# Optimization experiments

Hardware: AMD Instinct MI355X
Metric: run time of the kernel (lower is better)

The kernel has to match this reference:

```python
import jax, jax.numpy as jnp
import numpy as np

ALPHA = 1.702  # sigmoid-GLU scale
LIMIT = 7.0    # clamp limit
TOP_K = 2      # num_experts_per_tok


def setup_inputs() -> dict:
    key = jax.random.key(0)
    ks = jax.random.split(key, 4)
    B, S, H, E, I = 2, 1024, 1024, 8, 2048
    return {
        "hidden_states": jax.random.normal(ks[0], (B, S, H), jnp.float32),
        "router_weight": jax.random.normal(ks[1], (E, H), jnp.float32),
        "router_bias": jnp.zeros((E,), jnp.float32),
        "gate_up_proj": jax.random.normal(ks[2], (E, H, 2 * I), jnp.float32) * 0.02,
        "gate_up_bias": jnp.zeros((E, 2 * I), jnp.float32),
        "down_proj": jax.random.normal(ks[3], (E, I, H), jnp.float32) * 0.02,
        "down_bias": jnp.zeros((E, H), jnp.float32),
    }


def reference(hidden_states, router_weight, router_bias, gate_up_proj,
              gate_up_bias, down_proj, down_bias):
    B, S, H = hidden_states.shape
    E, _, two_I = gate_up_proj.shape
    I = two_I // 2

    flat = hidden_states.reshape(B * S, H)  # [T, H]

    # Router: softmax + top-k
    logits = flat @ router_weight.T + router_bias            # [T, E]
    scores = jax.nn.softmax(logits, axis=-1)
    topk_w, topk_idx = jax.lax.top_k(scores, TOP_K)          # [T, K]

    # Dense per-expert gated FFN (einsum 'abmh,ehn->abemn' computes all experts
    # on all tokens; the reshape/permute dance is a mathematical no-op).
    gu = jnp.einsum('th,ehn->ten', flat, gate_up_proj) + gate_up_bias  # [T, E, 2I]
    gate = jnp.minimum(gu[..., :I], LIMIT)
    up = jnp.clip(gu[..., I:], -LIMIT, LIMIT)
    glu = gate * jax.nn.sigmoid(gate * ALPHA)
    act = (up + 1.0) * glu                                   # [T, E, I]

    down = jnp.einsum('tei,eih->teh', act, down_proj) + down_bias  # [T, E, H]

    # Combine: gather each token's top-k expert outputs, weighted sum.
    gathered = jnp.take_along_axis(down, topk_idx[:, :, None], axis=1)  # [T, K, H]
    out = (gathered * topk_w[:, :, None]).sum(axis=1)        # [T, H]
    return out.reshape(B, S, H)
```

## Files before the change

kernel.cpp:

```cpp
#include <hip/hip_runtime.h>
#include <math.h>

#define TT 2048
#define HH 1024
#define EE 8
#define II 2048
#define N1 4096
#define ALPHA 1.702f
#define LIMIT 7.0f

typedef __attribute__((ext_vector_type(8))) short short8;
typedef __attribute__((ext_vector_type(4))) float floatx4;
typedef __attribute__((ext_vector_type(4))) unsigned int uintx4;

__device__ __forceinline__ short f2bf(float f) {
  union { float f; unsigned u; } v; v.f = f;
  unsigned r = (v.u + 0x7fffu + ((v.u >> 16) & 1u)) >> 16;
  return (short)r;
}
__device__ __forceinline__ float bf2f(unsigned short s) {
  union { unsigned u; float f; } v; v.u = ((unsigned)s) << 16;
  return v.f;
}
__device__ __forceinline__ unsigned cvt2(float lo, float hi) {
  unsigned r;
  asm("v_cvt_pk_bf16_f32 %0, %1, %2" : "=v"(r) : "v"(lo), "v"(hi));
  return r;
}

__global__ __launch_bounds__(256) void router_kernel(
    const float* __restrict__ x, const float* __restrict__ rw,
    const float* __restrict__ rb, int* __restrict__ topk_idx,
    float* __restrict__ topk_w) {
  const int t = blockIdx.x;
  const float* xr = x + (size_t)t * HH;
  const int lane = threadIdx.x & 63;
  const int wave = threadIdx.x >> 6;
  float xv[16];
#pragma unroll
  for (int i = 0; i < 16; i++) xv[i] = xr[lane + i * 64];
  __shared__ float logits[EE];
#pragma unroll
  for (int ee = 0; ee < 2; ee++) {
    const int e = wave * 2 + ee;
    const float* wr = rw + (size_t)e * HH;
    float s = 0.f;
#pragma unroll
    for (int i = 0; i < 16; i++) s += xv[i] * wr[lane + i * 64];
#pragma unroll
    for (int off = 32; off > 0; off >>= 1) s += __shfl_down(s, off, 64);
    if (lane == 0) logits[e] = s + rb[e];
  }
  __syncthreads();
  if (threadIdx.x == 0) {
    float l[EE], sc[EE];
    float mx = -3.4e38f;
    for (int i = 0; i < EE; i++) { l[i] = logits[i]; mx = fmaxf(mx, l[i]); }
    float sum = 0.f;
    for (int i = 0; i < EE; i++) { sc[i] = expf(l[i] - mx); sum += sc[i]; }
    const float inv = 1.f / sum;
    int i0 = 0;
    for (int i = 1; i < EE; i++) if (sc[i] > sc[i0]) i0 = i;
    int i1 = (i0 == 0) ? 1 : 0;
    for (int i = 0; i < EE; i++) if (i != i0 && sc[i] > sc[i1]) i1 = i;
    topk_idx[t * 2 + 0] = i0;
    topk_idx[t * 2 + 1] = i1;
    topk_w[t * 2 + 0] = sc[i0] * inv;
    topk_w[t * 2 + 1] = sc[i1] * inv;
  }
}

__global__ void assign_kernel(const int* __restrict__ topk_idx,
                              int* __restrict__ counts, int* __restrict__ rows) {
  const int id = blockIdx.x * blockDim.x + threadIdx.x;
  if (id >= TT * 2) return;
  const int e = topk_idx[id];
  const int slot = atomicAdd(&counts[e], 1);
  rows[e * TT + slot] = id;
}

__global__ __launch_bounds__(512, 4) void gemm_gu(
    const float* __restrict__ x, const float* __restrict__ gup,
    const float* __restrict__ gub, const int* __restrict__ counts,
    const int* __restrict__ rows, unsigned short* __restrict__ gu) {
  const int e = blockIdx.z, mtile = blockIdx.y, ntile = blockIdx.x;
  const int count = counts[e];
  if (mtile * 128 >= count) return;
  const int* rl = rows + e * TT + mtile * 128;
  __shared__ short As[128][40];
  __shared__ short Bs[128][40];
  const int tid = threadIdx.x;
  const int lane = tid & 63, wave = tid >> 6;
  const int wm = (wave & 1) << 6, wn = (wave >> 1) << 5;
  const int quad = lane >> 4, r16 = lane & 15;

  const int arow = tid >> 2, akoct = tid & 3;
  const int cr = (mtile * 128 + arow < count) ? arow : (count - 1 - mtile * 128);
  const float* ap = x + (size_t)(rl[cr] >> 1) * HH + akoct * 8;

  const int bn = tid & 127, bko = tid >> 7;
  const float* bp = gup + (size_t)e * HH * N1 + (size_t)bko * 8 * N1 + ntile * 128 + bn;

  floatx4 acc[4][2] = {};

  float4 va0 = ((const float4*)ap)[0];
  float4 va1 = ((const float4*)ap)[1];
  float vb[8];
#pragma unroll
  for (int j = 0; j < 8; j++) vb[j] = bp[(size_t)j * N1];
  ap += 32;
  bp += (size_t)32 * N1;

  for (int k0 = 0; k0 < HH; k0 += 32) {
    __syncthreads();
    uintx4 aw, bw;
    aw[0] = cvt2(va0.x, va0.y); aw[1] = cvt2(va0.z, va0.w);
    aw[2] = cvt2(va1.x, va1.y); aw[3] = cvt2(va1.z, va1.w);
    bw[0] = cvt2(vb[0], vb[1]); bw[1] = cvt2(vb[2], vb[3]);
    bw[2] = cvt2(vb[4], vb[5]); bw[3] = cvt2(vb[6], vb[7]);
    *(uintx4*)&As[arow][akoct * 8] = aw;
    *(uintx4*)&Bs[bn][bko * 8] = bw;
    if (k0 + 32 < HH) {
      va0 = ((const float4*)ap)[0];
      va1 = ((const float4*)ap)[1];
#pragma unroll
      for (int j = 0; j < 8; j++) vb[j] = bp[(size_t)j * N1];
      ap += 32;
      bp += (size_t)32 * N1;
    }
    __syncthreads();
    short8 af[4], bf_[2];
#pragma unroll
    for (int i = 0; i < 4; i++)
      af[i] = *(const short8*)&As[wm + i * 16 + r16][quad * 8];
#pragma unroll
    for (int j = 0; j < 2; j++)
      bf_[j] = *(const short8*)&Bs[wn + j * 16 + r16][quad * 8];
#pragma unroll
    for (int i = 0; i < 4; i++)
#pragma unroll
      for (int j = 0; j < 2; j++)
        acc[i][j] = __builtin_amdgcn_mfma_f32_16x16x32_bf16(af[i], bf_[j], acc[i][j], 0, 0, 0);
  }
#pragma unroll
  for (int i = 0; i < 4; i++) {
#pragma unroll
    for (int reg = 0; reg < 4; reg++) {
      const int rrow = wm + i * 16 + quad * 4 + reg;
      if (mtile * 128 + rrow < count) {
        const int ent = rl[rrow];
        unsigned short* orow = gu + (size_t)ent * N1 + ntile * 128;
#pragma unroll
        for (int j = 0; j < 2; j++) {
          const int c = wn + j * 16 + r16;
          const float v = acc[i][j][reg] + gub[e * N1 + ntile * 128 + c];
          orow[c] = (unsigned short)f2bf(v);
        }
      }
    }
  }
}

__global__ void act_kernel(const unsigned short* __restrict__ gu,
                           unsigned short* __restrict__ act) {
  const int id = blockIdx.x * blockDim.x + threadIdx.x;
  const int r = id >> 8;
  const int i8 = (id & 255) * 8;
  short8 g8 = *(const short8*)(gu + (size_t)r * N1 + i8);
  short8 u8 = *(const short8*)(gu + (size_t)r * N1 + II + i8);
  short8 o;
#pragma unroll
  for (int j = 0; j < 8; j++) {
    float g = bf2f((unsigned short)g8[j]);
    float u = bf2f((unsigned short)u8[j]);
    g = fminf(g, LIMIT);
    u = fminf(fmaxf(u, -LIMIT), LIMIT);
    const float glu = g / (1.f + expf(-g * ALPHA));
    o[j] = f2bf((u + 1.f) * glu);
  }
  *(short8*)(act + (size_t)r * II + i8) = o;
}

__global__ __launch_bounds__(512, 4) void gemm_down(
    const unsigned short* __restrict__ act, const float* __restrict__ dp,
    const float* __restrict__ db, const int* __restrict__ counts,
    const int* __restrict__ rows, float* __restrict__ dout0,
    float* __restrict__ dout1) {
  const int e = blockIdx.z >> 1, kc = blockIdx.z & 1;
  const int mtile = blockIdx.y, ntile = blockIdx.x;
  const int count = counts[e];
  if (mtile * 128 >= count) return;
  const int kb = kc * (II / 2);
  const int* rl = rows + e * TT + mtile * 128;
  __shared__ short As[128][40];
  __shared__ short Bs[128][40];
  const int tid = threadIdx.x;
  const int lane = tid & 63, wave = tid >> 6;
  const int wm = (wave & 1) << 6, wn = (wave >> 1) << 5;
  const int quad = lane >> 4, r16 = lane & 15;

  const int arow = tid >> 2, akoct = tid & 3;
  const int cr = (mtile * 128 + arow < count) ? arow : (count - 1 - mtile * 128);
  const unsigned short* ap = act + (size_t)rl[cr] * II + kb + akoct * 8;

  const int bn = tid & 127, bko = tid >> 7;
  const float* bp = dp + (size_t)e * II * HH + (size_t)(kb + bko * 8) * HH + ntile * 128 + bn;

  floatx4 acc[4][2] = {};

  short8 va = *(const short8*)ap;
  float vb[8];
#pragma unroll
  for (int j = 0; j < 8; j++) vb[j] = bp[(size_t)j * HH];
  ap += 32;
  bp += (size_t)32 * HH;

  for (int k0 = 0; k0 < II / 2; k0 += 32) {
    __syncthreads();
    uintx4 bw;
    bw[0] = cvt2(vb[0], vb[1]); bw[1] = cvt2(vb[2], vb[3]);
    bw[2] = cvt2(vb[4], vb[5]); bw[3] = cvt2(vb[6], vb[7]);
    *(short8*)&As[arow][akoct * 8] = va;
    *(uintx4*)&Bs[bn][bko * 8] = bw;
    if (k0 + 32 < II / 2) {
      va = *(const short8*)ap;
#pragma unroll
      for (int j = 0; j < 8; j++) vb[j] = bp[(size_t)j * HH];
      ap += 32;
      bp += (size_t)32 * HH;
    }
    __syncthreads();
    short8 af[4], bf_[2];
#pragma unroll
    for (int i = 0; i < 4; i++)
      af[i] = *(const short8*)&As[wm + i * 16 + r16][quad * 8];
#pragma unroll
    for (int j = 0; j < 2; j++)
      bf_[j] = *(const short8*)&Bs[wn + j * 16 + r16][quad * 8];
#pragma unroll
    for (int i = 0; i < 4; i++)
#pragma unroll
      for (int j = 0; j < 2; j++)
        acc[i][j] = __builtin_amdgcn_mfma_f32_16x16x32_bf16(af[i], bf_[j], acc[i][j], 0, 0, 0);
  }
  float* dc = kc ? dout1 : dout0;
#pragma unroll
  for (int i = 0; i < 4; i++) {
#pragma unroll
    for (int reg = 0; reg < 4; reg++) {
      const int rrow = wm + i * 16 + quad * 4 + reg;
      if (mtile * 128 + rrow < count) {
        const int ent = rl[rrow];
        float* orow = dc + (size_t)ent * HH + ntile * 128;
#pragma unroll
        for (int j = 0; j < 2; j++) {
          const int c = wn + j * 16 + r16;
          float v = acc[i][j][reg];
          if (kc == 0) v += db[e * HH + ntile * 128 + c];
          orow[c] = v;
        }
      }
    }
  }
}

__global__ void combine_kernel(const float* __restrict__ d0,
                               const float* __restrict__ d1,
                               const float* __restrict__ tw,
                               float* __restrict__ out) {
  const int id = blockIdx.x * blockDim.x + threadIdx.x;
  const int t = id >> 8;
  const int h = (id & 255) * 4;
  const float w0 = tw[t * 2], w1 = tw[t * 2 + 1];
  const size_t r0 = (size_t)(2 * t) * HH + h;
  const size_t r1 = (size_t)(2 * t + 1) * HH + h;
  const float4 a0 = *(const float4*)(d0 + r0);
  const float4 a1 = *(const float4*)(d1 + r0);
  const float4 b0 = *(const float4*)(d0 + r1);
  const float4 b1 = *(const float4*)(d1 + r1);
  float4 o;
  o.x = w0 * (a0.x + a1.x) + w1 * (b0.x + b1.x);
  o.y = w0 * (a0.y + a1.y) + w1 * (b0.y + b1.y);
  o.z = w0 * (a0.z + a1.z) + w1 * (b0.z + b1.z);
  o.w = w0 * (a0.w + a1.w) + w1 * (b0.w + b1.w);
  *(float4*)(out + (size_t)t * HH + h) = o;
}

extern "C" void kernel_launch(void* const* d_in, const int* in_sizes, int n_in,
                              void* d_out, int out_size, void* d_ws, size_t ws_size,
                              hipStream_t stream) {
  const float* x   = (const float*)d_in[0];
  const float* rw  = (const float*)d_in[1];
  const float* rb  = (const float*)d_in[2];
  const float* gup = (const float*)d_in[3];
  const float* gub = (const float*)d_in[4];
  const float* dp  = (const float*)d_in[5];
  const float* db  = (const float*)d_in[6];
  float* out = (float*)d_out;

  char* ws = (char*)d_ws;
  int*   topk_idx = (int*)(ws + 0);
  float* topk_w   = (float*)(ws + 16384);
  int*   counts   = (int*)(ws + 32768);
  int*   rows     = (int*)(ws + 33024);
  unsigned short* gu  = (unsigned short*)(ws + 131072);
  unsigned short* act = (unsigned short*)(ws + 131072 + 33554432);
  float* dout0 = (float*)(ws + 131072 + 33554432 + 16777216);
  float* dout1 = (float*)(ws + 131072);

  router_kernel<<<TT, 256, 0, stream>>>(x, rw, rb, topk_idx, topk_w);
  hipMemsetAsync(counts, 0, 64, stream);
  assign_kernel<<<(TT * 2 + 255) / 256, 256, 0, stream>>>(topk_idx, counts, rows);
  gemm_gu<<<dim3(N1 / 128, TT / 128, EE), 512, 0, stream>>>(x, gup, gub, counts, rows, gu);
  act_kernel<<<(TT * 2 * II / 8) / 256, 256, 0, stream>>>(gu, act);
  gemm_down<<<dim3(HH / 128, TT / 128, EE * 2), 512, 0, stream>>>(act, dp, db, counts, rows, dout0, dout1);
  combine_kernel<<<(TT * HH / 4) / 256, 256, 0, stream>>>(dout0, dout1, topk_w, out);
}
```

Before: 399.7 us.

## Fuse GLU activation into gate/up GEMM and double-buffer LDS in both GEMMs

The gate/up GEMM now tiles matching gate and up columns together, 64 of each per block, so each block can apply the clamp, sigmoid-GLU and bf16 conversion in its epilogue. This removes the separate activation kernel and the bf16 gate/up intermediate round-trip through global memory. Both GEMMs also gain double-buffered LDS with one barrier per half-step, lighter lgkmcnt barriers and s_setprio around the MFMA bursts, to overlap global loads with compute. The cost is more LDS per block and more live registers, which may lower occupancy.

```diff
diff --git a/kernel.cpp b/kernel.cpp
--- a/kernel.cpp
+++ b/kernel.cpp
@@ -27,6 +27,8 @@
   asm("v_cvt_pk_bf16_f32 %0, %1, %2" : "=v"(r) : "v"(lo), "v"(hi));
   return r;
 }
+
+#define LDS_BARRIER() asm volatile("s_waitcnt lgkmcnt(0)\ns_barrier" ::: "memory")
 
 __global__ __launch_bounds__(256) void router_kernel(
     const float* __restrict__ x, const float* __restrict__ rw,
@@ -79,69 +81,104 @@
   rows[e * TT + slot] = id;
 }
 
-__global__ __launch_bounds__(512, 4) void gemm_gu(
+__global__ __launch_bounds__(512, 4) void gemm_gu_fused(
     const float* __restrict__ x, const float* __restrict__ gup,
     const float* __restrict__ gub, const int* __restrict__ counts,
-    const int* __restrict__ rows, unsigned short* __restrict__ gu) {
+    const int* __restrict__ rows, unsigned short* __restrict__ act) {
   const int e = blockIdx.z, mtile = blockIdx.y, ntile = blockIdx.x;
   const int count = counts[e];
   if (mtile * 128 >= count) return;
   const int* rl = rows + e * TT + mtile * 128;
-  __shared__ short As[128][40];
-  __shared__ short Bs[128][40];
+  __shared__ short As[2][128][40];
+  __shared__ short Bg[2][64][40];
+  __shared__ short Bu[2][64][40];
   const int tid = threadIdx.x;
   const int lane = tid & 63, wave = tid >> 6;
-  const int wm = (wave & 1) << 6, wn = (wave >> 1) << 5;
+  const int wm = (wave & 1) << 6, wn = (wave >> 1) << 4;
   const int quad = lane >> 4, r16 = lane & 15;
 
   const int arow = tid >> 2, akoct = tid & 3;
   const int cr = (mtile * 128 + arow < count) ? arow : (count - 1 - mtile * 128);
-  const float* ap = x + (size_t)(rl[cr] >> 1) * HH + akoct * 8;
-
-  const int bn = tid & 127, bko = tid >> 7;
-  const float* bp = gup + (size_t)e * HH * N1 + (size_t)bko * 8 * N1 + ntile * 128 + bn;
-
-  floatx4 acc[4][2] = {};
-
-  float4 va0 = ((const float4*)ap)[0];
-  float4 va1 = ((const float4*)ap)[1];
-  float vb[8];
-#pragma unroll
-  for (int j = 0; j < 8; j++) vb[j] = bp[(size_t)j * N1];
-  ap += 32;
-  bp += (size_t)32 * N1;
-
-  for (int k0 = 0; k0 < HH; k0 += 32) {
-    __syncthreads();
-    uintx4 aw, bw;
-    aw[0] = cvt2(va0.x, va0.y); aw[1] = cvt2(va0.z, va0.w);
-    aw[2] = cvt2(va1.x, va1.y); aw[3] = cvt2(va1.z, va1.w);
-    bw[0] = cvt2(vb[0], vb[1]); bw[1] = cvt2(vb[2], vb[3]);
-    bw[2] = cvt2(vb[4], vb[5]); bw[3] = cvt2(vb[6], vb[7]);
-    *(uintx4*)&As[arow][akoct * 8] = aw;
-    *(uintx4*)&Bs[bn][bko * 8] = bw;
-    if (k0 + 32 < HH) {
-      va0 = ((const float4*)ap)[0];
-      va1 = ((const float4*)ap)[1];
-#pragma unroll
-      for (int j = 0; j < 8; j++) vb[j] = bp[(size_t)j * N1];
-      ap += 32;
-      bp += (size_t)32 * N1;
+  const float* abase = x + (size_t)(rl[cr] >> 1) * HH + akoct * 8;
+
+  const int half = tid >> 8;
+  const int bn = tid & 63, bko = (tid >> 6) & 3;
+  const float* bbase = gup + (size_t)e * HH * N1 + (size_t)(bko * 8) * N1 +
+                       (size_t)half * II + ntile * 64 + bn;
+  short* bdst0 = half ? &Bu[0][bn][bko * 8] : &Bg[0][bn][bko * 8];
+  short* bdst1 = half ? &Bu[1][bn][bko * 8] : &Bg[1][bn][bko * 8];
+
+  floatx4 acc_g[4] = {{0.f,0.f,0.f,0.f},{0.f,0.f,0.f,0.f},{0.f,0.f,0.f,0.f},{0.f,0.f,0.f,0.f}};
+  floatx4 acc_u[4] = {{0.f,0.f,0.f,0.f},{0.f,0.f,0.f,0.f},{0.f,0.f,0.f,0.f},{0.f,0.f,0.f,0.f}};
+
+  const float* apA = abase;
+  const float* apB = abase + 32;
+  const float* bpA = bbase;
+  const float* bpB = bbase + (size_t)32 * N1;
+
+  float4 vaA0, vaA1, vaB0, vaB1;
+  float vbA0, vbA1, vbA2, vbA3, vbA4, vbA5, vbA6, vbA7;
+  float vbB0, vbB1, vbB2, vbB3, vbB4, vbB5, vbB6, vbB7;
+
+#define GU_LOADA() do { \
+  vaA0 = ((const float4*)apA)[0]; vaA1 = ((const float4*)apA)[1]; \
+  vbA0 = bpA[0]; vbA1 = bpA[(size_t)1 * N1]; vbA2 = bpA[(size_t)2 * N1]; vbA3 = bpA[(size_t)3 * N1]; \
+  vbA4 = bpA[(size_t)4 * N1]; vbA5 = bpA[(size_t)5 * N1]; vbA6 = bpA[(size_t)6 * N1]; vbA7 = bpA[(size_t)7 * N1]; \
+  apA += 64; bpA += (size_t)64 * N1; } while (0)
+#define GU_LOADB() do { \
+  vaB0 = ((const float4*)apB)[0]; vaB1 = ((const float4*)apB)[1]; \
+  vbB0 = bpB[0]; vbB1 = bpB[(size_t)1 * N1]; vbB2 = bpB[(size_t)2 * N1]; vbB3 = bpB[(size_t)3 * N1]; \
+  vbB4 = bpB[(size_t)4 * N1]; vbB5 = bpB[(size_t)5 * N1]; vbB6 = bpB[(size_t)6 * N1]; vbB7 = bpB[(size_t)7 * N1]; \
+  apB += 64; bpB += (size_t)64 * N1; } while (0)
+#define GU_CVTW(buf, va0, va1, b0, b1, b2, b3, b4, b5, b6, b7) do { \
+  uintx4 aw, bw; \
+  aw[0] = cvt2(va0.x, va0.y); aw[1] = cvt2(va0.z, va0.w); \
+  aw[2] = cvt2(va1.x, va1.y); aw[3] = cvt2(va1.z, va1.w); \
+  bw[0] = cvt2(b0, b1); bw[1] = cvt2(b2, b3); \
+  bw[2] = cvt2(b4, b5); bw[3] = cvt2(b6, b7); \
+  *(uintx4*)&As[buf][arow][akoct * 8] = aw; \
+  *(uintx4*)((buf) ? bdst1 : bdst0) = bw; } while (0)
+#define GU_MMA(buf) do { \
+  short8 af0 = *(const short8*)&As[buf][wm + 0 * 16 + r16][quad * 8]; \
+  short8 af1 = *(const short8*)&As[buf][wm + 1 * 16 + r16][quad * 8]; \
+  short8 af2 = *(const short8*)&As[buf][wm + 2 * 16 + r16][quad * 8]; \
+  short8 af3 = *(const short8*)&As[buf][wm + 3 * 16 + r16][quad * 8]; \
+  short8 bgf = *(const short8*)&Bg[buf][wn + r16][quad * 8]; \
+  short8 buf_ = *(const short8*)&Bu[buf][wn + r16][quad * 8]; \
+  __builtin_amdgcn_s_setprio(1); \
+  acc_g[0] = __builtin_amdgcn_mfma_f32_16x16x32_bf16(af0, bgf, acc_g[0], 0, 0, 0); \
+  acc_u[0] = __builtin_amdgcn_mfma_f32_16x16x32_bf16(af0, buf_, acc_u[0], 0, 0, 0); \
+  acc_g[1] = __builtin_amdgcn_mfma_f32_16x16x32_bf16(af1, bgf, acc_g[1], 0, 0, 0); \
+  acc_u[1] = __builtin_amdgcn_mfma_f32_16x16x32_bf16(af1, buf_, acc_u[1], 0, 0, 0); \
+  acc_g[2] = __builtin_amdgcn_mfma_f32_16x16x32_bf16(af2, bgf, acc_g[2], 0, 0, 0); \
+  acc_u[2] = __builtin_amdgcn_mfma_f32_16x16x32_bf16(af2, buf_, acc_u[2], 0, 0, 0); \
+  acc_g[3] = __builtin_amdgcn_mfma_f32_16x16x32_bf16(af3, bgf, acc_g[3], 0, 0, 0); \
+  acc_u[3] = __builtin_amdgcn_mfma_f32_16x16x32_bf16(af3, buf_, acc_u[3], 0, 0, 0); \
+  __builtin_amdgcn_s_setprio(0); } while (0)
+
+  GU_LOADA();
+  GU_LOADB();
+  GU_CVTW(0, vaA0, vaA1, vbA0, vbA1, vbA2, vbA3, vbA4, vbA5, vbA6, vbA7);
+  GU_LOADA();
+
+  const int NT = HH / 32;
+#pragma unroll 1
+  for (int t = 0; t < NT; t += 2) {
+    LDS_BARRIER();
+    GU_CVTW(1, vaB0, vaB1, vbB0, vbB1, vbB2, vbB3, vbB4, vbB5, vbB6, vbB7);
+    if (t + 3 < NT) GU_LOADB();
+    GU_MMA(0);
+    LDS_BARRIER();
+    if (t + 2 < NT) {
+      GU_CVTW(0, vaA0, vaA1, vbA0, vbA1, vbA2, vbA3, vbA4, vbA5, vbA6, vbA7);
+      if (t + 4 < NT) GU_LOADA();
     }
-    __syncthreads();
-    short8 af[4], bf_[2];
-#pragma unroll
-    for (int i = 0; i < 4; i++)
-      af[i] = *(const short8*)&As[wm + i * 16 + r16][quad * 8];
-#pragma unroll
-    for (int j = 0; j < 2; j++)
-      bf_[j] = *(const short8*)&Bs[wn + j * 16 + r16][quad * 8];
-#pragma unroll
-    for (int i = 0; i < 4; i++)
-#pragma unroll
-      for (int j = 0; j < 2; j++)
-        acc[i][j] = __builtin_amdgcn_mfma_f32_16x16x32_bf16(af[i], bf_[j], acc[i][j], 0, 0, 0);
-  }
+    GU_MMA(1);
+  }
+
+  const int nc = ntile * 64 + wn + r16;
+  const float bg_bias = gub[e * N1 + nc];
+  const float bu_bias = gub[e * N1 + II + nc];
 #pragma unroll
   for (int i = 0; i < 4; i++) {
 #pragma unroll
@@ -149,36 +186,19 @@
       const int rrow = wm + i * 16 + quad * 4 + reg;
       if (mtile * 128 + rrow < count) {
         const int ent = rl[rrow];
-        unsigned short* orow = gu + (size_t)ent * N1 + ntile * 128;
-#pragma unroll
-        for (int j = 0; j < 2; j++) {
-          const int c = wn + j * 16 + r16;
-          const float v = acc[i][j][reg] + gub[e * N1 + ntile * 128 + c];
-          orow[c] = (unsigned short)f2bf(v);
-        }
+        float g = acc_g[i][reg] + bg_bias;
+        float u = acc_u[i][reg] + bu_bias;
+        g = fminf(g, LIMIT);
+        u = fminf(fmaxf(u, -LIMIT), LIMIT);
+        const float glu = g / (1.f + expf(-g * ALPHA));
+        act[(size_t)ent * II + nc] = (unsigned short)f2bf((u + 1.f) * glu);
       }
     }
   }
-}
-
-__global__ void act_kernel(const unsigned short* __restrict__ gu,
-                           unsigned short* __restrict__ act) {
-  const int id = blockIdx.x * blockDim.x + threadIdx.x;
-  const int r = id >> 8;
-  const int i8 = (id & 255) * 8;
-  short8 g8 = *(const short8*)(gu + (size_t)r * N1 + i8);
-  short8 u8 = *(const short8*)(gu + (size_t)r * N1 + II + i8);
-  short8 o;
-#pragma unroll
-  for (int j = 0; j < 8; j++) {
-    float g = bf2f((unsigned short)g8[j]);
-    float u = bf2f((unsigned short)u8[j]);
-    g = fminf(g, LIMIT);
-    u = fminf(fmaxf(u, -LIMIT), LIMIT);
-    const float glu = g / (1.f + expf(-g * ALPHA));
-    o[j] = f2bf((u + 1.f) * glu);
-  }
-  *(short8*)(act + (size_t)r * II + i8) = o;
+#undef GU_LOADA
+#undef GU_LOADB
+#undef GU_CVTW
+#undef GU_MMA
 }
 
 __global__ __launch_bounds__(512, 4) void gemm_down(
@@ -192,8 +212,8 @@
   if (mtile * 128 >= count) return;
   const int kb = kc * (II / 2);
   const int* rl = rows + e * TT + mtile * 128;
-  __shared__ short As[128][40];
-  __shared__ short Bs[128][40];
+  __shared__ short As[2][128][40];
+  __shared__ short Bs[2][128][40];
   const int tid = threadIdx.x;
   const int lane = tid & 63, wave = tid >> 6;
   const int wm = (wave & 1) << 6, wn = (wave >> 1) << 5;
@@ -201,48 +221,77 @@
 
   const int arow = tid >> 2, akoct = tid & 3;
   const int cr = (mtile * 128 + arow < count) ? arow : (count - 1 - mtile * 128);
-  const unsigned short* ap = act + (size_t)rl[cr] * II + kb + akoct * 8;
+  const unsigned short* abase = act + (size_t)rl[cr] * II + kb + akoct * 8;
 
   const int bn = tid & 127, bko = tid >> 7;
-  const float* bp = dp + (size_t)e * II * HH + (size_t)(kb + bko * 8) * HH + ntile * 128 + bn;
+  const float* bbase = dp + (size_t)e * II * HH + (size_t)(kb + bko * 8) * HH +
+                       ntile * 128 + bn;
 
   floatx4 acc[4][2] = {};
 
-  short8 va = *(const short8*)ap;
-  float vb[8];
-#pragma unroll
-  for (int j = 0; j < 8; j++) vb[j] = bp[(size_t)j * HH];
-  ap += 32;
-  bp += (size_t)32 * HH;
-
-  for (int k0 = 0; k0 < II / 2; k0 += 32) {
-    __syncthreads();
-    uintx4 bw;
-    bw[0] = cvt2(vb[0], vb[1]); bw[1] = cvt2(vb[2], vb[3]);
-    bw[2] = cvt2(vb[4], vb[5]); bw[3] = cvt2(vb[6], vb[7]);
-    *(short8*)&As[arow][akoct * 8] = va;
-    *(uintx4*)&Bs[bn][bko * 8] = bw;
-    if (k0 + 32 < II / 2) {
-      va = *(const short8*)ap;
-#pragma unroll
-      for (int j = 0; j < 8; j++) vb[j] = bp[(size_t)j * HH];
-      ap += 32;
-      bp += (size_t)32 * HH;
+  const unsigned short* apA = abase;
+  const unsigned short* apB = abase + 32;
+  const float* bpA = bbase;
+  const float* bpB = bbase + (size_t)32 * HH;
+
+  short8 svA, svB;
+  float vbA0, vbA1, vbA2, vbA3, vbA4, vbA5, vbA6, vbA7;
+  float vbB0, vbB1, vbB2, vbB3, vbB4, vbB5, vbB6, vbB7;
+
+#define DN_LOADA() do { \
+  svA = *(const short8*)apA; \
+  vbA0 = bpA[0]; vbA1 = bpA[(size_t)1 * HH]; vbA2 = bpA[(size_t)2 * HH]; vbA3 = bpA[(size_t)3 * HH]; \
+  vbA4 = bpA[(size_t)4 * HH]; vbA5 = bpA[(size_t)5 * HH]; vbA6 = bpA[(size_t)6 * HH]; vbA7 = bpA[(size_t)7 * HH]; \
+  apA += 64; bpA += (size_t)64 * HH; } while (0)
+#define DN_LOADB() do { \
+  svB = *(const short8*)apB; \
+  vbB0 = bpB[0]; vbB1 = bpB[(size_t)1 * HH]; vbB2 = bpB[(size_t)2 * HH]; vbB3 = bpB[(size_t)3 * HH]; \
+  vbB4 = bpB[(size_t)4 * HH]; vbB5 = bpB[(size_t)5 * HH]; vbB6 = bpB[(size_t)6 * HH]; vbB7 = bpB[(size_t)7 * HH]; \
+  apB += 64; bpB += (size_t)64 * HH; } while (0)
+#define DN_CVTW(buf, sv, b0, b1, b2, b3, b4, b5, b6, b7) do { \
+  uintx4 bw; \
+  bw[0] = cvt2(b0, b1); bw[1] = cvt2(b2, b3); \
+  bw[2] = cvt2(b4, b5); bw[3] = cvt2(b6, b7); \
+  *(short8*)&As[buf][arow][akoct * 8] = sv; \
+  *(uintx4*)&Bs[buf][bn][bko * 8] = bw; } while (0)
+#define DN_MMA(buf) do { \
+  short8 af0 = *(const short8*)&As[buf][wm + 0 * 16 + r16][quad * 8]; \
+  short8 af1 = *(const short8*)&As[buf][wm + 1 * 16 + r16][quad * 8]; \
+  short8 af2 = *(const short8*)&As[buf][wm + 2 * 16 + r16][quad * 8]; \
+  short8 af3 = *(const short8*)&As[buf][wm + 3 * 16 + r16][quad * 8]; \
+  short8 bf0 = *(const short8*)&Bs[buf][wn + 0 * 16 + r16][quad * 8]; \
+  short8 bf1 = *(const short8*)&Bs[buf][wn + 1 * 16 + r16][quad * 8]; \
+  __builtin_amdgcn_s_setprio(1); \
+  acc[0][0] = __builtin_amdgcn_mfma_f32_16x16x32_bf16(af0, bf0, acc[0][0], 0, 0, 0); \
+  acc[0][1] = __builtin_amdgcn_mfma_f32_16x16x32_bf16(af0, bf1, acc[0][1], 0, 0, 0); \
+  acc[1][0] = __builtin_amdgcn_mfma_f32_16x16x32_bf16(af1, bf0, acc[1][0], 0, 0, 0); \
+  acc[1][1] = __builtin_amdgcn_mfma_f32_16x16x32_bf16(af1, bf1, acc[1][1], 0, 0, 0); \
+  acc[2][0] = __builtin_amdgcn_mfma_f32_16x16x32_bf16(af2, bf0, acc[2][0], 0, 0, 0); \
+  acc[2][1] = __builtin_amdgcn_mfma_f32_16x16x32_bf16(af2, bf1, acc[2][1], 0, 0, 0); \
+  acc[3][0] = __builtin_amdgcn_mfma_f32_16x16x32_bf16(af3, bf0, acc[3][0], 0, 0, 0); \
+  acc[3][1] = __builtin_amdgcn_mfma_f32_16x16x32_bf16(af3, bf1, acc[3][1], 0, 0, 0); \
+  __builtin_amdgcn_s_setprio(0); } while (0)
+
+  DN_LOADA();
+  DN_LOADB();
+  DN_CVTW(0, svA, vbA0, vbA1, vbA2, vbA3, vbA4, vbA5, vbA6, vbA7);
+  DN_LOADA();
+
+  const int NT = (II / 2) / 32;
+#pragma unroll 1
+  for (int t = 0; t < NT; t += 2) {
+    LDS_BARRIER();
+    DN_CVTW(1, svB, vbB0, vbB1, vbB2, vbB3, vbB4, vbB5, vbB6, vbB7);
+    if (t + 3 < NT) DN_LOADB();
+    DN_MMA(0);
+    LDS_BARRIER();
+    if (t + 2 < NT) {
+      DN_CVTW(0, svA, vbA0, vbA1, vbA2, vbA3, vbA4, vbA5, vbA6, vbA7);
+      if (t + 4 < NT) DN_LOADA();
     }
-    __syncthreads();
-    short8 af[4], bf_[2];
-#pragma unroll
-    for (int i = 0; i < 4; i++)
-      af[i] = *(const short8*)&As[wm + i * 16 + r16][quad * 8];
-#pragma unroll
-    for (int j = 0; j < 2; j++)
-      bf_[j] = *(const short8*)&Bs[wn + j * 16 + r16][quad * 8];
-#pragma unroll
-    for (int i = 0; i < 4; i++)
-#pragma unroll
-      for (int j = 0; j < 2; j++)
-        acc[i][j] = __builtin_amdgcn_mfma_f32_16x16x32_bf16(af[i], bf_[j], acc[i][j], 0, 0, 0);
-  }
+    DN_MMA(1);
+  }
+
   float* dc = kc ? dout1 : dout0;
 #pragma unroll
   for (int i = 0; i < 4; i++) {
@@ -262,6 +311,10 @@
       }
     }
   }
+#undef DN_LOADA
+#undef DN_LOADB
+#undef DN_CVTW
+#undef DN_MMA
 }
 
 __global__ void combine_kernel(const float* __restrict__ d0,
@@ -303,16 +356,14 @@
   float* topk_w   = (float*)(ws + 16384);
   int*   counts   = (int*)(ws + 32768);
   int*   rows     = (int*)(ws + 33024);
-  unsigned short* gu  = (unsigned short*)(ws + 131072);
-  unsigned short* act = (unsigned short*)(ws + 131072 + 33554432);
-  float* dout0 = (float*)(ws + 131072 + 33554432 + 16777216);
-  float* dout1 = (float*)(ws + 131072);
+  unsigned short* act = (unsigned short*)(ws + 131072);
+  float* dout0 = (float*)(ws + 131072 + 16777216);
+  float* dout1 = (float*)(ws + 131072 + 2 * 16777216);
 
   router_kernel<<<TT, 256, 0, stream>>>(x, rw, rb, topk_idx, topk_w);
   hipMemsetAsync(counts, 0, 64, stream);
   assign_kernel<<<(TT * 2 + 255) / 256, 256, 0, stream>>>(topk_idx, counts, rows);
-  gemm_gu<<<dim3(N1 / 128, TT / 128, EE), 512, 0, stream>>>(x, gup, gub, counts, rows, gu);
-  act_kernel<<<(TT * 2 * II / 8) / 256, 256, 0, stream>>>(gu, act);
+  gemm_gu_fused<<<dim3(II / 64, TT / 128, EE), 512, 0, stream>>>(x, gup, gub, counts, rows, act);
   gemm_down<<<dim3(HH / 128, TT / 128, EE * 2), 512, 0, stream>>>(act, dp, db, counts, rows, dout0, dout1);
   combine_kernel<<<(TT * HH / 4) / 256, 256, 0, stream>>>(dout0, dout1, topk_w, out);
 }
```

Result: no change. 400.1 us (+0.1%).
